# Kernel tuning notes

Hardware: AMD Instinct MI355X
Metric: run time of the kernel (lower is better)

Reference implementation:

```python
import jax, jax.numpy as jnp
import numpy as np

L_F, D_F = 32, 16      # fast window / hop
L_S, D_S = 32, 16      # slow window / hop
H = 32                 # SSM hidden dim
GH = 64                # GRU hidden dim
N_GRU = 4


def setup_inputs() -> dict:
    key = jax.random.key(0)
    ks = jax.random.split(key, 16)
    B, T = 2, 64000
    s = 0.1
    return {
        "x": jax.random.normal(ks[0], (B, T), jnp.float32),
        # slow branch input FC (1 -> GH), stored as (in, out)
        "slow_in_W": jax.random.normal(ks[1], (1, GH), jnp.float32) * s,
        "slow_in_b": jax.random.normal(ks[2], (GH,), jnp.float32) * s,
        # 4 stacked GRU layers, torch gate order [r, z, n], stored (in, 3*GH)
        "gru_Wih": jax.random.normal(ks[3], (N_GRU, GH, 3 * GH), jnp.float32) * s,
        "gru_Whh": jax.random.normal(ks[4], (N_GRU, GH, 3 * GH), jnp.float32) * s,
        "gru_bih": jax.random.normal(ks[5], (N_GRU, 3 * GH), jnp.float32) * s,
        "gru_bhh": jax.random.normal(ks[6], (N_GRU, 3 * GH), jnp.float32) * s,
        # slow branch output FC (GH -> GH)
        "slow_out_W": jax.random.normal(ks[7], (GH, GH), jnp.float32) * s,
        "slow_out_b": jax.random.normal(ks[8], (GH,), jnp.float32) * s,
        # slow_to_ssm (GH -> 2H)
        "s2s_W": jax.random.normal(ks[9], (GH, 2 * H), jnp.float32) * s,
        "s2s_b": jax.random.normal(ks[10], (2 * H,), jnp.float32) * s,
        # fast branch F_IN (1 -> H) and F_OUT (H -> 1)
        "fin_W": jax.random.normal(ks[11], (1, H), jnp.float32) * s,
        "fin_b": jax.random.normal(ks[12], (H,), jnp.float32) * s,
        "fout_W": jax.random.normal(ks[13], (H, 1), jnp.float32) * s,
        "fout_b": jax.random.normal(ks[14], (1,), jnp.float32) * s,
    }


def _forward(x, slow_in_W, slow_in_b, gru_Wih, gru_Whh, gru_bih, gru_bhh,
             slow_out_W, slow_out_b, s2s_W, s2s_b, fin_W, fin_b, fout_W, fout_b):
    B, T = x.shape
    nf = (T - L_F) // D_F + 1   # fast frame count
    ns = (T - L_S) // D_S + 1   # slow frame count
    fidx = jnp.arange(nf)[:, None] * D_F + jnp.arange(L_F)[None, :]  # (nf, L_F)
    sidx = jnp.arange(ns)[:, None] * D_S + jnp.arange(L_S)[None, :]  # (ns, L_S)
    frames = x[:, fidx]                                  # (B, nf, L_F)  == x.unfold

    BS = B * ns
    xs = x[:, sidx].reshape(BS, L_S, 1)
    h = jax.nn.relu(xs @ slow_in_W + slow_in_b)          # (BS, L_S, GH)
    for l in range(N_GRU):
        Whh, bhh = gru_Whh[l], gru_bhh[l]
        xg = h @ gru_Wih[l] + gru_bih[l]                 # (BS, L_S, 3GH)

        def step(hc, xg_t, Whh=Whh, bhh=bhh):
            hg = hc @ Whh + bhh
            r = jax.nn.sigmoid(xg_t[:, :GH] + hg[:, :GH])
            z = jax.nn.sigmoid(xg_t[:, GH:2 * GH] + hg[:, GH:2 * GH])
            n = jnp.tanh(xg_t[:, 2 * GH:] + r * hg[:, 2 * GH:])
            hn = (1.0 - z) * n + z * hc
            return hn, hn

        _, seq = jax.lax.scan(step, jnp.zeros((BS, GH), x.dtype), jnp.swapaxes(xg, 0, 1))
        h = jax.nn.relu(jnp.swapaxes(seq, 0, 1))         # (BS, L_S, GH)
    slow_feat = h[:, -1, :] @ slow_out_W + slow_out_b    # (BS, GH)

    # ---- modulation parameters ----
    eps = (slow_feat @ s2s_W + s2s_b).reshape(B, ns, 2 * H)
    A_s = jax.nn.sigmoid(eps[..., :H])                   # (B, ns, H)
    g_s = eps[..., H:]
    delta = D_S // D_F
    A_flat = jnp.repeat(A_s, delta, axis=1)[:, :nf].reshape(B * nf, H)
    g_flat = jnp.repeat(g_s, delta, axis=1)[:, :nf].reshape(B * nf, H)

    # ---- fast branch: diagonal SSM h_t = A*h_{t-1} + g * F_IN(x_t) ----
    ff = frames.reshape(B * nf, L_F, 1)
    x_emb = (ff @ fin_W + fin_b) * g_flat[:, None, :]    # (B*nf, L_F, H)

    def ssm_step(hc, xt):
        hn = A_flat * hc + xt
        return hn, hn

    _, hall = jax.lax.scan(ssm_step, jnp.zeros((B * nf, H), x.dtype),
                           jnp.swapaxes(x_emb, 0, 1))
    hall = jnp.swapaxes(hall, 0, 1)                      # (B*nf, L_F, H)
    s_hat = (hall @ fout_W + fout_b)[..., 0].reshape(B, nf, L_F)

    # ---- overlap-add (F.fold) ----
    out = jnp.zeros((B, T), x.dtype).at[:, fidx].add(s_hat)
    return out


def reference(x, slow_in_W, slow_in_b, gru_Wih, gru_Whh, gru_bih, gru_bhh,
              slow_out_W, slow_out_b, s2s_W, s2s_b, fin_W, fin_b, fout_W, fout_b):
    return _forward(x, slow_in_W, slow_in_b, gru_Wih, gru_Whh, gru_bih, gru_bhh,
                    slow_out_W, slow_out_b, s2s_W, s2s_b, fin_W, fin_b, fout_W, fout_b)
```

## Files before the change

kernel.cpp:

```cpp
#include <hip/hip_runtime.h>

#define GH 64
#define LS 32
#define HF 32
#define DS 16

#define NLOG2E -1.4426950408889634f
#define P2LOG2E 2.8853900817779268f

typedef short bf16x8 __attribute__((ext_vector_type(8)));
typedef float f32x4 __attribute__((ext_vector_type(4)));

#define MFMA16(a, b, c) __builtin_amdgcn_mfma_f32_16x16x32_bf16(a, b, c, 0, 0, 0)

__device__ __forceinline__ unsigned int f2bf_rne(float f) {
    unsigned int u = __float_as_uint(f);
    return (u + 0x7FFFu + ((u >> 16) & 1u)) >> 16;
}
__device__ __forceinline__ unsigned short f2bf_h(float f) {
    return (unsigned short)((__float_as_uint(f) + 0x8000u) >> 16);
}
__device__ __forceinline__ unsigned int pack_trunc(float v0, float v1) {
    return __builtin_amdgcn_perm(__float_as_uint(v1), __float_as_uint(v0),
                                 0x07060302u);
}
__device__ __forceinline__ bf16x8 as_frag(uint4 u) {
    union { uint4 a; bf16x8 b; } cv; cv.a = u; return cv.b;
}

__device__ __forceinline__ bf16x8 ld_afrag(const unsigned short* slot, int m,
                                           int quad, int half) {
    int b   = half * 4 + quad;
    int idx = (m << 6) + ((b ^ (m & 7)) << 3);
    return as_frag(*reinterpret_cast<const uint4*>(slot + idx));
}

__global__ __launch_bounds__(256) void prep_weights(
    const float* __restrict__ Wih, const float* __restrict__ Whh,
    const float* __restrict__ soW, const float* __restrict__ s2sW,
    unsigned short* __restrict__ wsW,
    float* __restrict__ out, int out_n)
{
    int gid = blockIdx.x * 256 + threadIdx.x;
    int nthreads = gridDim.x * 256;

    {
        float4* out4 = reinterpret_cast<float4*>(out);
        int n4 = out_n >> 2;
        for (int i = gid; i < n4; i += nthreads)
            out4[i] = make_float4(0.f, 0.f, 0.f, 0.f);
        int tail = out_n & 3;
        if (gid < tail) out[n4 * 4 + gid] = 0.0f;
    }

    if (gid >= 104 * 1024) return;

    float v;
    int dest;
    if (gid < 98304) {
        int g     = gid % 192;
        int r1    = gid / 192;
        int k     = r1 & 63;
        int r2    = r1 >> 6;
        int l     = r2 & 3;
        int which = r2 >> 2;
        int m3  = g / 64;
        int col = g - m3 * 64;
        const float* W = which ? Whh : Wih;
        v = W[(size_t)l * GH * 192 + k * 192 + g];
        v *= (m3 == 2) ? P2LOG2E : NLOG2E;
        int jt = col >> 4, c = col & 15;
        int mat  = which * 3 + m3;
        int rest = (l * 6 + mat) * 4 + jt;
        int kc = k >> 5, j = k & 7, lane = ((k >> 3) & 3) * 16 + c;
        dest = rest * 1024 + kc * 512 + lane * 8 + j;
    } else {
        int e   = gid - 98304;
        int col = e & 63;
        int k   = (e >> 6) & 63;
        int m2  = e >> 12;
        v = (m2 ? s2sW : soW)[k * 64 + col];
        if (m2 && col < 32) v *= NLOG2E;
        int jt = col >> 4, c = col & 15;
        int rest = 96 + m2 * 4 + jt;
        int kc = k >> 5, j = k & 7, lane = ((k >> 3) & 3) * 16 + c;
        dest = rest * 1024 + kc * 512 + lane * 8 + j;
    }
    wsW[dest] = (unsigned short)f2bf_rne(v);
}

__global__ __launch_bounds__(256, 2) void slowfast_fused(
    const float* __restrict__ x,
    const float* __restrict__ siW,  const float* __restrict__ sib,
    const float* __restrict__ bih,  const float* __restrict__ bhh,
    const float* __restrict__ sob,  const float* __restrict__ s2sb,
    const float* __restrict__ finW, const float* __restrict__ finb,
    const float* __restrict__ foutW, const float* __restrict__ foutb,
    const unsigned short* __restrict__ wsW,
    float* __restrict__ out,
    int T, int ns, int BS)
{
    __shared__ __align__(16) unsigned short hseq[LS * 16 * 64];
    __shared__ __align__(16) unsigned short hrec[2 * 16 * 64];
    __shared__ float xs[16 * 33];
    __shared__ float AG[16 * 65];

    const int tid  = threadIdx.x;
    const int lane = tid & 63;
    const int jt   = tid >> 6;
    const int c    = lane & 15;
    const int quad = lane >> 4;
    const int col  = jt * 16 + c;
    const int seqbase = blockIdx.x * 16;
    const uint4* wf = reinterpret_cast<const uint4*>(wsW);

    for (int p = tid; p < 512; p += 256) {
        int seq = p >> 5, t = p & 31;
        int q = seqbase + seq; if (q > BS - 1) q = BS - 1;
        int b  = (q >= ns) ? 1 : 0;
        int si = q - b * ns;
        xs[seq * 33 + t] = x[b * T + si * DS + t];
    }
    __syncthreads();

    {
        int chp = tid & 31;
        int grp = tid >> 5;
        int ch  = chp << 1;
        float w0 = siW[ch], w1 = siW[ch + 1];
        float b0 = sib[ch], b1 = sib[ch + 1];
        #pragma unroll 4
        for (int it = 0; it < 64; ++it) {
            int p = grp + (it << 3);
            int s = p >> 5, t = p & 31;
            float xv = xs[s * 33 + t];
            float v0 = fmaxf(fmaf(xv, w0, b0), 0.0f);
            float v1 = fmaxf(fmaf(xv, w1, b1), 0.0f);
            int idx = (t << 10) + (s << 6) + ((((ch >> 3) ^ (s & 7))) << 3) + (ch & 7);
            *reinterpret_cast<unsigned int*>(&hseq[idx]) = pack_trunc(v0, v1);
        }
    }

    int wIdx[4];
    #pragma unroll
    for (int i = 0; i < 4; ++i) {
        int row = quad * 4 + i;
        wIdx[i] = (row << 6) + ((((col >> 3) ^ (row & 7))) << 3) + (col & 7);
    }

    __syncthreads();

    bf16x8 a0 = ld_afrag(hseq, c, quad, 0);
    bf16x8 a1 = ld_afrag(hseq, c, quad, 1);

    for (int l = 0; l < 4; ++l) {
        bf16x8 BiR[2], BiZ[2], BiN[2], BhR[2], BhZ[2], BhN[2];
        #pragma unroll
        for (int kc = 0; kc < 2; ++kc) {
            int base = (l * 6 * 4 + jt) * 128 + kc * 64 + lane;
            BiR[kc] = as_frag(wf[base]);
            BiZ[kc] = as_frag(wf[base + 512]);
            BiN[kc] = as_frag(wf[base + 1024]);
            BhR[kc] = as_frag(wf[base + 1536]);
            BhZ[kc] = as_frag(wf[base + 2048]);
            BhN[kc] = as_frag(wf[base + 2560]);
        }
        float bRs  = NLOG2E  * (bih[l * 192 + col]      + bhh[l * 192 + col]);
        float bZs  = NLOG2E  * (bih[l * 192 + 64 + col] + bhh[l * 192 + 64 + col]);
        float bNIs = P2LOG2E * bih[l * 192 + 128 + col];
        float bNHs = P2LOG2E * bhh[l * 192 + 128 + col];
        const f32x4 vbR  = (f32x4){bRs,  bRs,  bRs,  bRs};
        const f32x4 vbZ  = (f32x4){bZs,  bZs,  bZs,  bZs};
        const f32x4 vbNI = (f32x4){bNIs, bNIs, bNIs, bNIs};
        const f32x4 vbNH = (f32x4){bNHs, bNHs, bNHs, bNHs};

        float hprev[4] = {0.0f, 0.0f, 0.0f, 0.0f};
        const bool storeSeq = (l != 3);

        #pragma unroll 2
        for (int t = 0; t < LS; ++t) {
            f32x4 aR  = MFMA16(a0, BiR[0], vbR);
            f32x4 aZ  = MFMA16(a0, BiZ[0], vbZ);
            f32x4 aNI = MFMA16(a0, BiN[0], vbNI);
            aR  = MFMA16(a1, BiR[1], aR);
            aZ  = MFMA16(a1, BiZ[1], aZ);
            aNI = MFMA16(a1, BiN[1], aNI);
            f32x4 aNH = vbNH;
            if (t > 0) {
                const unsigned short* hb = hrec + (((t - 1) & 1) << 10);
                bf16x8 h0 = ld_afrag(hb, c, quad, 0);
                bf16x8 h1 = ld_afrag(hb, c, quad, 1);
                aR  = MFMA16(h0, BhR[0], aR);
                aZ  = MFMA16(h0, BhZ[0], aZ);
                aNH = MFMA16(h0, BhN[0], aNH);
                aR  = MFMA16(h1, BhR[1], aR);
                aZ  = MFMA16(h1, BhZ[1], aZ);
                aNH = MFMA16(h1, BhN[1], aNH);
            }
            unsigned short* wb = hseq + (t << 10);
            unsigned short* wr = hrec + ((t & 1) << 10);
            const bool doSeq = storeSeq || (t == 31);
            #pragma unroll
            for (int i = 0; i < 4; ++i) {
                float r  = __builtin_amdgcn_rcpf(1.0f + __builtin_amdgcn_exp2f(aR[i]));
                float z  = __builtin_amdgcn_rcpf(1.0f + __builtin_amdgcn_exp2f(aZ[i]));
                float e  = __builtin_amdgcn_exp2f(fmaf(r, aNH[i], aNI[i]));
                float n  = fmaf(-2.0f, __builtin_amdgcn_rcpf(e + 1.0f), 1.0f);
                float hn = fmaf(z, hprev[i] - n, n);
                hprev[i] = hn;
                wr[wIdx[i]] = f2bf_h(hn);
                if (doSeq)
                    wb[wIdx[i]] = f2bf_h(fmaxf(hn, 0.0f));
            }
            const unsigned short* nb = hseq + (((t + 1) & 31) << 10);
            a0 = ld_afrag(nb, c, quad, 0);
            a1 = ld_afrag(nb, c, quad, 1);
            __syncthreads();
        }
    }

    {
        bf16x8 e0 = ld_afrag(hseq + (31 << 10), c, quad, 0);
        bf16x8 e1 = ld_afrag(hseq + (31 << 10), c, quad, 1);
        bf16x8 Bso[2], Bs2[2];
        #pragma unroll
        for (int kc = 0; kc < 2; ++kc) {
            Bso[kc] = as_frag(wf[(96 + jt)  * 128 + kc * 64 + lane]);
            Bs2[kc] = as_frag(wf[(100 + jt) * 128 + kc * 64 + lane]);
        }
        float sb = sob[col];
        f32x4 accS = (f32x4){sb, sb, sb, sb};
        accS = MFMA16(e0, Bso[0], accS);
        accS = MFMA16(e1, Bso[1], accS);
        #pragma unroll
        for (int i = 0; i < 4; ++i)
            hseq[wIdx[i]] = f2bf_h(accS[i]);
        __syncthreads();
        bf16x8 s0 = ld_afrag(hseq, c, quad, 0);
        bf16x8 s1 = ld_afrag(hseq, c, quad, 1);
        float eb = (jt < 2) ? NLOG2E * s2sb[col] : s2sb[col];
        f32x4 accE = (f32x4){eb, eb, eb, eb};
        accE = MFMA16(s0, Bs2[0], accE);
        accE = MFMA16(s1, Bs2[1], accE);
        #pragma unroll
        for (int i = 0; i < 4; ++i) {
            int row = quad * 4 + i;
            float v = accE[i];
            AG[row * 65 + col] = (jt < 2)
                ? __builtin_amdgcn_rcpf(1.0f + __builtin_amdgcn_exp2f(v)) : v;
        }
    }
    __syncthreads();
    {
        int fch = tid & 31;
        float Gfw = finW[fch], Gbw = finb[fch], cFo = foutW[fch], cfb = foutb[0];
        #pragma unroll
        for (int half = 0; half < 2; ++half) {
            int frame = half * 8 + (tid >> 5);
            int q = seqbase + frame;
            if (q < BS) {
                int b  = (q >= ns) ? 1 : 0;
                int fi = q - b * ns;
                float cA = AG[frame * 65 + fch];
                float cG = AG[frame * 65 + 32 + fch];
                float Gf = Gfw * cG;
                float Gb = Gbw * cG;
                float h = 0.0f;
                const float* xrow = xs + frame * 33;
                float* op = out + (size_t)b * T + fi * DS;
                #pragma unroll 1
                for (int t = 0; t < LS; ++t) {
                    h = fmaf(cA, h, fmaf(xrow[t], Gf, Gb));
                    float s = h * cFo;
                    s += __shfl_xor(s, 1);
                    s += __shfl_xor(s, 2);
                    s += __shfl_xor(s, 4);
                    s += __shfl_xor(s, 8);
                    s += __shfl_xor(s, 16);
                    if (fch == 0) atomicAdd(&op[t], s + cfb);
                }
            }
        }
    }
}

extern "C" void kernel_launch(void* const* d_in, const int* in_sizes, int n_in,
                              void* d_out, int out_size, void* d_ws, size_t ws_size,
                              hipStream_t stream)
{
    (void)n_in; (void)ws_size;
    const float* x     = (const float*)d_in[0];
    const float* siW   = (const float*)d_in[1];
    const float* sib   = (const float*)d_in[2];
    const float* Wih   = (const float*)d_in[3];
    const float* Whh   = (const float*)d_in[4];
    const float* bih   = (const float*)d_in[5];
    const float* bhh   = (const float*)d_in[6];
    const float* soW   = (const float*)d_in[7];
    const float* sob   = (const float*)d_in[8];
    const float* s2sW  = (const float*)d_in[9];
    const float* s2sb  = (const float*)d_in[10];
    const float* finW  = (const float*)d_in[11];
    const float* finb  = (const float*)d_in[12];
    const float* foutW = (const float*)d_in[13];
    const float* foutb = (const float*)d_in[14];

    int T  = in_sizes[0] / 2;
    int ns = (T - LS) / DS + 1;
    int BS = 2 * ns;

    unsigned short* wsW = (unsigned short*)d_ws;

    prep_weights<<<dim3(416), dim3(256), 0, stream>>>(
        Wih, Whh, soW, s2sW, wsW, (float*)d_out, out_size);

    slowfast_fused<<<dim3((BS + 15) / 16), dim3(256), 0, stream>>>(
        x, siW, sib, bih, bhh, sob, s2sb, finW, finb, foutW, foutb,
        wsW, (float*)d_out, T, ns, BS);
}
```

Baseline: 172.6 us.

## Move GRU sequence buffer from LDS to global workspace for higher occupancy

Adds a templated path that keeps the per-block 32-step hidden-sequence buffer (64 KB) in global workspace memory instead of shared memory, which frees LDS so the launch bound can request 4 blocks per CU instead of 2. The last-layer conditional store is removed, so every step is written. The cost is that each recurrent step now reads and writes activations through the global/L2 path instead of LDS, adding latency on the serial recurrence. It falls back to the LDS version when the workspace is too small.

```diff
diff --git a/kernel.cpp b/kernel.cpp
--- a/kernel.cpp
+++ b/kernel.cpp
@@ -28,7 +28,8 @@
     union { uint4 a; bf16x8 b; } cv; cv.a = u; return cv.b;
 }
 
-__device__ __forceinline__ bf16x8 ld_afrag(const unsigned short* slot, int m,
+template <typename P>
+__device__ __forceinline__ bf16x8 ld_afrag(const P* slot, int m,
                                            int quad, int half) {
     int b   = half * 4 + quad;
     int idx = (m << 6) + ((b ^ (m & 7)) << 3);
@@ -89,7 +90,8 @@
     wsW[dest] = (unsigned short)f2bf_rne(v);
 }
 
-__global__ __launch_bounds__(256, 2) void slowfast_fused(
+template <bool GHSEQ>
+__global__ __launch_bounds__(256, GHSEQ ? 4 : 2) void slowfast_fused(
     const float* __restrict__ x,
     const float* __restrict__ siW,  const float* __restrict__ sib,
     const float* __restrict__ bih,  const float* __restrict__ bhh,
@@ -97,10 +99,11 @@
     const float* __restrict__ finW, const float* __restrict__ finb,
     const float* __restrict__ foutW, const float* __restrict__ foutb,
     const unsigned short* __restrict__ wsW,
+    unsigned short* __restrict__ hsg,
     float* __restrict__ out,
     int T, int ns, int BS)
 {
-    __shared__ __align__(16) unsigned short hseq[LS * 16 * 64];
+    __shared__ __align__(16) unsigned short hseq_l[GHSEQ ? 64 : LS * 16 * 64];
     __shared__ __align__(16) unsigned short hrec[2 * 16 * 64];
     __shared__ float xs[16 * 33];
     __shared__ float AG[16 * 65];
@@ -113,6 +116,9 @@
     const int col  = jt * 16 + c;
     const int seqbase = blockIdx.x * 16;
     const uint4* wf = reinterpret_cast<const uint4*>(wsW);
+
+    unsigned short* hseq = GHSEQ ? (hsg + (size_t)blockIdx.x * (LS * 16 * 64))
+                                 : hseq_l;
 
     for (int p = tid; p < 512; p += 256) {
         int seq = p >> 5, t = p & 31;
@@ -175,7 +181,6 @@
         const f32x4 vbNH = (f32x4){bNHs, bNHs, bNHs, bNHs};
 
         float hprev[4] = {0.0f, 0.0f, 0.0f, 0.0f};
-        const bool storeSeq = (l != 3);
 
         #pragma unroll 2
         for (int t = 0; t < LS; ++t) {
@@ -199,7 +204,6 @@
             }
             unsigned short* wb = hseq + (t << 10);
             unsigned short* wr = hrec + ((t & 1) << 10);
-            const bool doSeq = storeSeq || (t == 31);
             #pragma unroll
             for (int i = 0; i < 4; ++i) {
                 float r  = __builtin_amdgcn_rcpf(1.0f + __builtin_amdgcn_exp2f(aR[i]));
@@ -209,8 +213,7 @@
                 float hn = fmaf(z, hprev[i] - n, n);
                 hprev[i] = hn;
                 wr[wIdx[i]] = f2bf_h(hn);
-                if (doSeq)
-                    wb[wIdx[i]] = f2bf_h(fmaxf(hn, 0.0f));
+                wb[wIdx[i]] = f2bf_h(fmaxf(hn, 0.0f));
             }
             const unsigned short* nb = hseq + (((t + 1) & 31) << 10);
             a0 = ld_afrag(nb, c, quad, 0);
@@ -288,7 +291,7 @@
                               void* d_out, int out_size, void* d_ws, size_t ws_size,
                               hipStream_t stream)
 {
-    (void)n_in; (void)ws_size;
+    (void)n_in;
     const float* x     = (const float*)d_in[0];
     const float* siW   = (const float*)d_in[1];
     const float* sib   = (const float*)d_in[2];
@@ -308,13 +311,23 @@
     int T  = in_sizes[0] / 2;
     int ns = (T - LS) / DS + 1;
     int BS = 2 * ns;
+    int nblocks = (BS + 15) / 16;
 
     unsigned short* wsW = (unsigned short*)d_ws;
 
     prep_weights<<<dim3(416), dim3(256), 0, stream>>>(
         Wih, Whh, soW, s2sW, wsW, (float*)d_out, out_size);
 
-    slowfast_fused<<<dim3((BS + 15) / 16), dim3(256), 0, stream>>>(
-        x, siW, sib, bih, bhh, sob, s2sb, finW, finb, foutW, foutb,
-        wsW, (float*)d_out, T, ns, BS);
-}
+    size_t need = (size_t)(4 << 20) + (size_t)nblocks * (LS * 16 * 64 * 2);
+    if (ws_size >= need) {
+        unsigned short* hsg =
+            (unsigned short*)((char*)d_ws + (4 << 20));
+        slowfast_fused<true><<<dim3(nblocks), dim3(256), 0, stream>>>(
+            x, siW, sib, bih, bhh, sob, s2sb, finW, finb, foutW, foutb,
+            wsW, hsg, (float*)d_out, T, ns, BS);
+    } else {
+        slowfast_fused<false><<<dim3(nblocks), dim3(256), 0, stream>>>(
+            x, siW, sib, bih, bhh, sob, s2sb, finW, finb, foutW, foutb,
+            wsW, nullptr, (float*)d_out, T, ns, BS);
+    }
+}
```

After: 201.0 us. +16.5%, slower.

## Pipeline four GRU layers as a wavefront across waves in 1024-thread blocks

Applied to the files above, without the earlier changes.

The four stacked GRU layers, previously run one after another by the same four waves, now each get four waves of a 1024-thread block. They run as a diagonal wavefront: layer l handles timestep tau-l, and activations pass through double-buffered LDS boundary tiles. This cuts the serial step count from 128 to 35 barrier-separated steps and drops the full 32-step hseq buffer, so LDS use shrinks. The input FC is computed per step directly into MFMA fragments. In exchange each barrier now syncs 16 waves, waves idle at the pipeline ends, and per-CU occupancy and register limits change with the larger block.

```diff
diff --git a/kernel.cpp b/kernel.cpp
--- a/kernel.cpp
+++ b/kernel.cpp
@@ -89,7 +89,7 @@
     wsW[dest] = (unsigned short)f2bf_rne(v);
 }
 
-__global__ __launch_bounds__(256, 2) void slowfast_fused(
+__global__ __launch_bounds__(1024, 4) void slowfast_fused(
     const float* __restrict__ x,
     const float* __restrict__ siW,  const float* __restrict__ sib,
     const float* __restrict__ bih,  const float* __restrict__ bhh,
@@ -100,46 +100,55 @@
     float* __restrict__ out,
     int T, int ns, int BS)
 {
-    __shared__ __align__(16) unsigned short hseq[LS * 16 * 64];
-    __shared__ __align__(16) unsigned short hrec[2 * 16 * 64];
+    __shared__ __align__(16) unsigned short bnd[3 * 2 * 1024];
+    __shared__ __align__(16) unsigned short hrec[4 * 2 * 1024];
+    __shared__ __align__(16) unsigned short hfin[1024];
     __shared__ float xs[16 * 33];
     __shared__ float AG[16 * 65];
+    __shared__ __align__(16) float swS[64], sbS[64];
 
     const int tid  = threadIdx.x;
     const int lane = tid & 63;
-    const int jt   = tid >> 6;
+    const int w    = tid >> 6;
+    const int l    = w >> 2;
+    const int jt   = w & 3;
     const int c    = lane & 15;
     const int quad = lane >> 4;
     const int col  = jt * 16 + c;
     const int seqbase = blockIdx.x * 16;
     const uint4* wf = reinterpret_cast<const uint4*>(wsW);
 
-    for (int p = tid; p < 512; p += 256) {
-        int seq = p >> 5, t = p & 31;
+    if (tid < 512) {
+        int seq = tid >> 5, t = tid & 31;
         int q = seqbase + seq; if (q > BS - 1) q = BS - 1;
         int b  = (q >= ns) ? 1 : 0;
         int si = q - b * ns;
         xs[seq * 33 + t] = x[b * T + si * DS + t];
-    }
-    __syncthreads();
-
-    {
-        int chp = tid & 31;
-        int grp = tid >> 5;
-        int ch  = chp << 1;
-        float w0 = siW[ch], w1 = siW[ch + 1];
-        float b0 = sib[ch], b1 = sib[ch + 1];
-        #pragma unroll 4
-        for (int it = 0; it < 64; ++it) {
-            int p = grp + (it << 3);
-            int s = p >> 5, t = p & 31;
-            float xv = xs[s * 33 + t];
-            float v0 = fmaxf(fmaf(xv, w0, b0), 0.0f);
-            float v1 = fmaxf(fmaf(xv, w1, b1), 0.0f);
-            int idx = (t << 10) + (s << 6) + ((((ch >> 3) ^ (s & 7))) << 3) + (ch & 7);
-            *reinterpret_cast<unsigned int*>(&hseq[idx]) = pack_trunc(v0, v1);
-        }
-    }
+    } else if (tid < 576) {
+        int i = tid - 512;
+        swS[i] = siW[i];
+        sbS[i] = sib[i];
+    }
+
+    bf16x8 BiR[2], BiZ[2], BiN[2], BhR[2], BhZ[2], BhN[2];
+    #pragma unroll
+    for (int kc = 0; kc < 2; ++kc) {
+        int base = (l * 24 + jt) * 128 + kc * 64 + lane;
+        BiR[kc] = as_frag(wf[base]);
+        BiZ[kc] = as_frag(wf[base + 512]);
+        BiN[kc] = as_frag(wf[base + 1024]);
+        BhR[kc] = as_frag(wf[base + 1536]);
+        BhZ[kc] = as_frag(wf[base + 2048]);
+        BhN[kc] = as_frag(wf[base + 2560]);
+    }
+    float bRs  = NLOG2E  * (bih[l * 192 + col]      + bhh[l * 192 + col]);
+    float bZs  = NLOG2E  * (bih[l * 192 + 64 + col] + bhh[l * 192 + 64 + col]);
+    float bNIs = P2LOG2E * bih[l * 192 + 128 + col];
+    float bNHs = P2LOG2E * bhh[l * 192 + 128 + col];
+    const f32x4 vbR  = (f32x4){bRs,  bRs,  bRs,  bRs};
+    const f32x4 vbZ  = (f32x4){bZs,  bZs,  bZs,  bZs};
+    const f32x4 vbNI = (f32x4){bNIs, bNIs, bNIs, bNIs};
+    const f32x4 vbNH = (f32x4){bNHs, bNHs, bNHs, bNHs};
 
     int wIdx[4];
     #pragma unroll
@@ -148,96 +157,108 @@
         wIdx[i] = (row << 6) + ((((col >> 3) ^ (row & 7))) << 3) + (col & 7);
     }
 
+    float hprev[4] = {0.0f, 0.0f, 0.0f, 0.0f};
+    const float4* sw4 = reinterpret_cast<const float4*>(swS);
+    const float4* sb4 = reinterpret_cast<const float4*>(sbS);
+
+    #pragma unroll 1
+    for (int tau = 0; tau < 35; ++tau) {
+        __syncthreads();
+        int t = tau - l;
+        if (t < 0 || t >= 32) continue;
+
+        bf16x8 a0, a1;
+        if (l == 0) {
+            float xv = xs[c * 33 + t];
+            float4 wA = sw4[quad * 2],     wB = sw4[quad * 2 + 1];
+            float4 bA = sb4[quad * 2],     bB = sb4[quad * 2 + 1];
+            float4 wC = sw4[8 + quad * 2], wD = sw4[8 + quad * 2 + 1];
+            float4 bC = sb4[8 + quad * 2], bD = sb4[8 + quad * 2 + 1];
+            uint4 u;
+            u.x = pack_trunc(fmaxf(fmaf(xv, wA.x, bA.x), 0.f),
+                             fmaxf(fmaf(xv, wA.y, bA.y), 0.f));
+            u.y = pack_trunc(fmaxf(fmaf(xv, wA.z, bA.z), 0.f),
+                             fmaxf(fmaf(xv, wA.w, bA.w), 0.f));
+            u.z = pack_trunc(fmaxf(fmaf(xv, wB.x, bB.x), 0.f),
+                             fmaxf(fmaf(xv, wB.y, bB.y), 0.f));
+            u.w = pack_trunc(fmaxf(fmaf(xv, wB.z, bB.z), 0.f),
+                             fmaxf(fmaf(xv, wB.w, bB.w), 0.f));
+            a0 = as_frag(u);
+            u.x = pack_trunc(fmaxf(fmaf(xv, wC.x, bC.x), 0.f),
+                             fmaxf(fmaf(xv, wC.y, bC.y), 0.f));
+            u.y = pack_trunc(fmaxf(fmaf(xv, wC.z, bC.z), 0.f),
+                             fmaxf(fmaf(xv, wC.w, bC.w), 0.f));
+            u.z = pack_trunc(fmaxf(fmaf(xv, wD.x, bD.x), 0.f),
+                             fmaxf(fmaf(xv, wD.y, bD.y), 0.f));
+            u.w = pack_trunc(fmaxf(fmaf(xv, wD.z, bD.z), 0.f),
+                             fmaxf(fmaf(xv, wD.w, bD.w), 0.f));
+            a1 = as_frag(u);
+        } else {
+            const unsigned short* src = bnd + (((l - 1) << 1) + (t & 1)) * 1024;
+            a0 = ld_afrag(src, c, quad, 0);
+            a1 = ld_afrag(src, c, quad, 1);
+        }
+
+        f32x4 aR  = MFMA16(a0, BiR[0], vbR);
+        f32x4 aZ  = MFMA16(a0, BiZ[0], vbZ);
+        f32x4 aNI = MFMA16(a0, BiN[0], vbNI);
+        aR  = MFMA16(a1, BiR[1], aR);
+        aZ  = MFMA16(a1, BiZ[1], aZ);
+        aNI = MFMA16(a1, BiN[1], aNI);
+        f32x4 aNH = vbNH;
+        if (t > 0) {
+            const unsigned short* hb = hrec + ((l << 1) + ((t - 1) & 1)) * 1024;
+            bf16x8 h0 = ld_afrag(hb, c, quad, 0);
+            bf16x8 h1 = ld_afrag(hb, c, quad, 1);
+            aR  = MFMA16(h0, BhR[0], aR);
+            aZ  = MFMA16(h0, BhZ[0], aZ);
+            aNH = MFMA16(h0, BhN[0], aNH);
+            aR  = MFMA16(h1, BhR[1], aR);
+            aZ  = MFMA16(h1, BhZ[1], aZ);
+            aNH = MFMA16(h1, BhN[1], aNH);
+        }
+        unsigned short* wr = hrec + ((l << 1) + (t & 1)) * 1024;
+        unsigned short* wb = (l < 3) ? (bnd + ((l << 1) + (t & 1)) * 1024)
+                                     : hfin;
+        #pragma unroll
+        for (int i = 0; i < 4; ++i) {
+            float r  = __builtin_amdgcn_rcpf(1.0f + __builtin_amdgcn_exp2f(aR[i]));
+            float z  = __builtin_amdgcn_rcpf(1.0f + __builtin_amdgcn_exp2f(aZ[i]));
+            float e  = __builtin_amdgcn_exp2f(fmaf(r, aNH[i], aNI[i]));
+            float n  = fmaf(-2.0f, __builtin_amdgcn_rcpf(e + 1.0f), 1.0f);
+            float hn = fmaf(z, hprev[i] - n, n);
+            hprev[i] = hn;
+            wr[wIdx[i]] = f2bf_h(hn);
+            wb[wIdx[i]] = f2bf_h(fmaxf(hn, 0.0f));
+        }
+    }
     __syncthreads();
 
-    bf16x8 a0 = ld_afrag(hseq, c, quad, 0);
-    bf16x8 a1 = ld_afrag(hseq, c, quad, 1);
-
-    for (int l = 0; l < 4; ++l) {
-        bf16x8 BiR[2], BiZ[2], BiN[2], BhR[2], BhZ[2], BhN[2];
-        #pragma unroll
-        for (int kc = 0; kc < 2; ++kc) {
-            int base = (l * 6 * 4 + jt) * 128 + kc * 64 + lane;
-            BiR[kc] = as_frag(wf[base]);
-            BiZ[kc] = as_frag(wf[base + 512]);
-            BiN[kc] = as_frag(wf[base + 1024]);
-            BhR[kc] = as_frag(wf[base + 1536]);
-            BhZ[kc] = as_frag(wf[base + 2048]);
-            BhN[kc] = as_frag(wf[base + 2560]);
-        }
-        float bRs  = NLOG2E  * (bih[l * 192 + col]      + bhh[l * 192 + col]);
-        float bZs  = NLOG2E  * (bih[l * 192 + 64 + col] + bhh[l * 192 + 64 + col]);
-        float bNIs = P2LOG2E * bih[l * 192 + 128 + col];
-        float bNHs = P2LOG2E * bhh[l * 192 + 128 + col];
-        const f32x4 vbR  = (f32x4){bRs,  bRs,  bRs,  bRs};
-        const f32x4 vbZ  = (f32x4){bZs,  bZs,  bZs,  bZs};
-        const f32x4 vbNI = (f32x4){bNIs, bNIs, bNIs, bNIs};
-        const f32x4 vbNH = (f32x4){bNHs, bNHs, bNHs, bNHs};
-
-        float hprev[4] = {0.0f, 0.0f, 0.0f, 0.0f};
-        const bool storeSeq = (l != 3);
-
-        #pragma unroll 2
-        for (int t = 0; t < LS; ++t) {
-            f32x4 aR  = MFMA16(a0, BiR[0], vbR);
-            f32x4 aZ  = MFMA16(a0, BiZ[0], vbZ);
-            f32x4 aNI = MFMA16(a0, BiN[0], vbNI);
-            aR  = MFMA16(a1, BiR[1], aR);
-            aZ  = MFMA16(a1, BiZ[1], aZ);
-            aNI = MFMA16(a1, BiN[1], aNI);
-            f32x4 aNH = vbNH;
-            if (t > 0) {
-                const unsigned short* hb = hrec + (((t - 1) & 1) << 10);
-                bf16x8 h0 = ld_afrag(hb, c, quad, 0);
-                bf16x8 h1 = ld_afrag(hb, c, quad, 1);
-                aR  = MFMA16(h0, BhR[0], aR);
-                aZ  = MFMA16(h0, BhZ[0], aZ);
-                aNH = MFMA16(h0, BhN[0], aNH);
-                aR  = MFMA16(h1, BhR[1], aR);
-                aZ  = MFMA16(h1, BhZ[1], aZ);
-                aNH = MFMA16(h1, BhN[1], aNH);
-            }
-            unsigned short* wb = hseq + (t << 10);
-            unsigned short* wr = hrec + ((t & 1) << 10);
-            const bool doSeq = storeSeq || (t == 31);
-            #pragma unroll
-            for (int i = 0; i < 4; ++i) {
-                float r  = __builtin_amdgcn_rcpf(1.0f + __builtin_amdgcn_exp2f(aR[i]));
-                float z  = __builtin_amdgcn_rcpf(1.0f + __builtin_amdgcn_exp2f(aZ[i]));
-                float e  = __builtin_amdgcn_exp2f(fmaf(r, aNH[i], aNI[i]));
-                float n  = fmaf(-2.0f, __builtin_amdgcn_rcpf(e + 1.0f), 1.0f);
-                float hn = fmaf(z, hprev[i] - n, n);
-                hprev[i] = hn;
-                wr[wIdx[i]] = f2bf_h(hn);
-                if (doSeq)
-                    wb[wIdx[i]] = f2bf_h(fmaxf(hn, 0.0f));
-            }
-            const unsigned short* nb = hseq + (((t + 1) & 31) << 10);
-            a0 = ld_afrag(nb, c, quad, 0);
-            a1 = ld_afrag(nb, c, quad, 1);
-            __syncthreads();
-        }
-    }
-
-    {
-        bf16x8 e0 = ld_afrag(hseq + (31 << 10), c, quad, 0);
-        bf16x8 e1 = ld_afrag(hseq + (31 << 10), c, quad, 1);
-        bf16x8 Bso[2], Bs2[2];
+    f32x4 accS;
+    bf16x8 Bso[2], Bs2[2];
+    if (w < 4) {
+        bf16x8 e0 = ld_afrag(hfin, c, quad, 0);
+        bf16x8 e1 = ld_afrag(hfin, c, quad, 1);
         #pragma unroll
         for (int kc = 0; kc < 2; ++kc) {
             Bso[kc] = as_frag(wf[(96 + jt)  * 128 + kc * 64 + lane]);
             Bs2[kc] = as_frag(wf[(100 + jt) * 128 + kc * 64 + lane]);
         }
         float sb = sob[col];
-        f32x4 accS = (f32x4){sb, sb, sb, sb};
+        accS = (f32x4){sb, sb, sb, sb};
         accS = MFMA16(e0, Bso[0], accS);
         accS = MFMA16(e1, Bso[1], accS);
+    }
+    __syncthreads();
+    if (w < 4) {
         #pragma unroll
         for (int i = 0; i < 4; ++i)
-            hseq[wIdx[i]] = f2bf_h(accS[i]);
-        __syncthreads();
-        bf16x8 s0 = ld_afrag(hseq, c, quad, 0);
-        bf16x8 s1 = ld_afrag(hseq, c, quad, 1);
+            hfin[wIdx[i]] = f2bf_h(accS[i]);
+    }
+    __syncthreads();
+    if (w < 4) {
+        bf16x8 s0 = ld_afrag(hfin, c, quad, 0);
+        bf16x8 s1 = ld_afrag(hfin, c, quad, 1);
         float eb = (jt < 2) ? NLOG2E * s2sb[col] : s2sb[col];
         f32x4 accE = (f32x4){eb, eb, eb, eb};
         accE = MFMA16(s0, Bs2[0], accE);
@@ -251,34 +272,32 @@
         }
     }
     __syncthreads();
-    {
-        int fch = tid & 31;
-        float Gfw = finW[fch], Gbw = finb[fch], cFo = foutW[fch], cfb = foutb[0];
-        #pragma unroll
-        for (int half = 0; half < 2; ++half) {
-            int frame = half * 8 + (tid >> 5);
-            int q = seqbase + frame;
-            if (q < BS) {
-                int b  = (q >= ns) ? 1 : 0;
-                int fi = q - b * ns;
-                float cA = AG[frame * 65 + fch];
-                float cG = AG[frame * 65 + 32 + fch];
-                float Gf = Gfw * cG;
-                float Gb = Gbw * cG;
-                float h = 0.0f;
-                const float* xrow = xs + frame * 33;
-                float* op = out + (size_t)b * T + fi * DS;
-                #pragma unroll 1
-                for (int t = 0; t < LS; ++t) {
-                    h = fmaf(cA, h, fmaf(xrow[t], Gf, Gb));
-                    float s = h * cFo;
-                    s += __shfl_xor(s, 1);
-                    s += __shfl_xor(s, 2);
-                    s += __shfl_xor(s, 4);
-                    s += __shfl_xor(s, 8);
-                    s += __shfl_xor(s, 16);
-                    if (fch == 0) atomicAdd(&op[t], s + cfb);
-                }
+    if (tid < 512) {
+        int fch   = tid & 31;
+        int frame = tid >> 5;
+        int q = seqbase + frame;
+        if (q < BS) {
+            float Gfw = finW[fch], Gbw = finb[fch];
+            float cFo = foutW[fch], cfb = foutb[0];
+            int b  = (q >= ns) ? 1 : 0;
+            int fi = q - b * ns;
+            float cA = AG[frame * 65 + fch];
+            float cG = AG[frame * 65 + 32 + fch];
+            float Gf = Gfw * cG;
+            float Gb = Gbw * cG;
+            float h = 0.0f;
+            const float* xrow = xs + frame * 33;
+            float* op = out + (size_t)b * T + fi * DS;
+            #pragma unroll 1
+            for (int t = 0; t < LS; ++t) {
+                h = fmaf(cA, h, fmaf(xrow[t], Gf, Gb));
+                float s = h * cFo;
+                s += __shfl_xor(s, 1);
+                s += __shfl_xor(s, 2);
+                s += __shfl_xor(s, 4);
+                s += __shfl_xor(s, 8);
+                s += __shfl_xor(s, 16);
+                if (fch == 0) atomicAdd(&op[t], s + cfb);
             }
         }
     }
@@ -308,13 +327,14 @@
     int T  = in_sizes[0] / 2;
     int ns = (T - LS) / DS + 1;
     int BS = 2 * ns;
+    int nblocks = (BS + 15) / 16;
 
     unsigned short* wsW = (unsigned short*)d_ws;
 
     prep_weights<<<dim3(416), dim3(256), 0, stream>>>(
         Wih, Whh, soW, s2sW, wsW, (float*)d_out, out_size);
 
-    slowfast_fused<<<dim3((BS + 15) / 16), dim3(256), 0, stream>>>(
+    slowfast_fused<<<dim3(nblocks), dim3(1024), 0, stream>>>(
         x, siW, sib, bih, bhh, sob, s2sb, finW, finb, foutW, foutb,
         wsW, (float*)d_out, T, ns, BS);
 }
```

After: 179.3 us. +3.9%, slower.

## Process two 16-sequence tiles per block to interleave independent GRU chains

Applied to the files above, without the earlier changes.

Each block now handles 32 slow sequences as two independent 16-row tiles (A and B), issuing their MFMAs and gate math interleaved so one tile's dependent chain can hide the other's latency. Doing this halves the number of blocks and per-step barriers per sequence, and the recurrent weight fragments are reused for twice the rows. In exchange it doubles LDS and register use, lowers occupancy (launch bounds change from 2 to 1), and always writes the layer-3 sequence to LDS even though only the last step is needed.

```diff
diff --git a/kernel.cpp b/kernel.cpp
--- a/kernel.cpp
+++ b/kernel.cpp
@@ -89,7 +89,25 @@
     wsW[dest] = (unsigned short)f2bf_rne(v);
 }
 
-__global__ __launch_bounds__(256, 2) void slowfast_fused(
+__device__ __forceinline__ void gate4(const f32x4& aR, const f32x4& aZ,
+                                      const f32x4& aNI, const f32x4& aNH,
+                                      float* hprev, unsigned short* wr,
+                                      unsigned short* wb, const int* wIdx)
+{
+    #pragma unroll
+    for (int i = 0; i < 4; ++i) {
+        float r  = __builtin_amdgcn_rcpf(1.0f + __builtin_amdgcn_exp2f(aR[i]));
+        float z  = __builtin_amdgcn_rcpf(1.0f + __builtin_amdgcn_exp2f(aZ[i]));
+        float e  = __builtin_amdgcn_exp2f(fmaf(r, aNH[i], aNI[i]));
+        float n  = fmaf(-2.0f, __builtin_amdgcn_rcpf(e + 1.0f), 1.0f);
+        float hn = fmaf(z, hprev[i] - n, n);
+        hprev[i] = hn;
+        wr[wIdx[i]] = f2bf_h(hn);
+        wb[wIdx[i]] = f2bf_h(fmaxf(hn, 0.0f));
+    }
+}
+
+__global__ __launch_bounds__(256, 1) void slowfast_fused(
     const float* __restrict__ x,
     const float* __restrict__ siW,  const float* __restrict__ sib,
     const float* __restrict__ bih,  const float* __restrict__ bhh,
@@ -100,10 +118,13 @@
     float* __restrict__ out,
     int T, int ns, int BS)
 {
-    __shared__ __align__(16) unsigned short hseq[LS * 16 * 64];
-    __shared__ __align__(16) unsigned short hrec[2 * 16 * 64];
-    __shared__ float xs[16 * 33];
-    __shared__ float AG[16 * 65];
+    __shared__ __align__(16) unsigned short hseq[2 * LS * 16 * 64];
+    __shared__ __align__(16) unsigned short hrec[2 * 2 * 16 * 64];
+    __shared__ float xs[32 * 33];
+    __shared__ float AG[32 * 65];
+
+    unsigned short* hseqA = hseq;
+    unsigned short* hseqB = hseq + LS * 16 * 64;
 
     const int tid  = threadIdx.x;
     const int lane = tid & 63;
@@ -111,10 +132,10 @@
     const int c    = lane & 15;
     const int quad = lane >> 4;
     const int col  = jt * 16 + c;
-    const int seqbase = blockIdx.x * 16;
+    const int seqbase = blockIdx.x * 32;
     const uint4* wf = reinterpret_cast<const uint4*>(wsW);
 
-    for (int p = tid; p < 512; p += 256) {
+    for (int p = tid; p < 1024; p += 256) {
         int seq = p >> 5, t = p & 31;
         int q = seqbase + seq; if (q > BS - 1) q = BS - 1;
         int b  = (q >= ns) ? 1 : 0;
@@ -133,11 +154,15 @@
         for (int it = 0; it < 64; ++it) {
             int p = grp + (it << 3);
             int s = p >> 5, t = p & 31;
+            int idx = (t << 10) + (s << 6) + ((((ch >> 3) ^ (s & 7))) << 3) + (ch & 7);
             float xv = xs[s * 33 + t];
-            float v0 = fmaxf(fmaf(xv, w0, b0), 0.0f);
-            float v1 = fmaxf(fmaf(xv, w1, b1), 0.0f);
-            int idx = (t << 10) + (s << 6) + ((((ch >> 3) ^ (s & 7))) << 3) + (ch & 7);
-            *reinterpret_cast<unsigned int*>(&hseq[idx]) = pack_trunc(v0, v1);
+            *reinterpret_cast<unsigned int*>(&hseqA[idx]) =
+                pack_trunc(fmaxf(fmaf(xv, w0, b0), 0.0f),
+                           fmaxf(fmaf(xv, w1, b1), 0.0f));
+            float xw = xs[(s + 16) * 33 + t];
+            *reinterpret_cast<unsigned int*>(&hseqB[idx]) =
+                pack_trunc(fmaxf(fmaf(xw, w0, b0), 0.0f),
+                           fmaxf(fmaf(xw, w1, b1), 0.0f));
         }
     }
 
@@ -150,8 +175,10 @@
 
     __syncthreads();
 
-    bf16x8 a0 = ld_afrag(hseq, c, quad, 0);
-    bf16x8 a1 = ld_afrag(hseq, c, quad, 1);
+    bf16x8 aA0 = ld_afrag(hseqA, c, quad, 0);
+    bf16x8 aA1 = ld_afrag(hseqA, c, quad, 1);
+    bf16x8 aB0 = ld_afrag(hseqB, c, quad, 0);
+    bf16x8 aB1 = ld_afrag(hseqB, c, quad, 1);
 
     for (int l = 0; l < 4; ++l) {
         bf16x8 BiR[2], BiZ[2], BiN[2], BhR[2], BhZ[2], BhN[2];
@@ -174,54 +201,60 @@
         const f32x4 vbNI = (f32x4){bNIs, bNIs, bNIs, bNIs};
         const f32x4 vbNH = (f32x4){bNHs, bNHs, bNHs, bNHs};
 
-        float hprev[4] = {0.0f, 0.0f, 0.0f, 0.0f};
-        const bool storeSeq = (l != 3);
+        float hprevA[4] = {0.0f, 0.0f, 0.0f, 0.0f};
+        float hprevB[4] = {0.0f, 0.0f, 0.0f, 0.0f};
 
         #pragma unroll 2
         for (int t = 0; t < LS; ++t) {
-            f32x4 aR  = MFMA16(a0, BiR[0], vbR);
-            f32x4 aZ  = MFMA16(a0, BiZ[0], vbZ);
-            f32x4 aNI = MFMA16(a0, BiN[0], vbNI);
-            aR  = MFMA16(a1, BiR[1], aR);
-            aZ  = MFMA16(a1, BiZ[1], aZ);
-            aNI = MFMA16(a1, BiN[1], aNI);
-            f32x4 aNH = vbNH;
+            f32x4 aRA  = MFMA16(aA0, BiR[0], vbR);
+            f32x4 aRB  = MFMA16(aB0, BiR[0], vbR);
+            f32x4 aZA  = MFMA16(aA0, BiZ[0], vbZ);
+            f32x4 aZB  = MFMA16(aB0, BiZ[0], vbZ);
+            f32x4 aNIA = MFMA16(aA0, BiN[0], vbNI);
+            f32x4 aNIB = MFMA16(aB0, BiN[0], vbNI);
+            aRA  = MFMA16(aA1, BiR[1], aRA);
+            aRB  = MFMA16(aB1, BiR[1], aRB);
+            aZA  = MFMA16(aA1, BiZ[1], aZA);
+            aZB  = MFMA16(aB1, BiZ[1], aZB);
+            aNIA = MFMA16(aA1, BiN[1], aNIA);
+            aNIB = MFMA16(aB1, BiN[1], aNIB);
+            f32x4 aNHA = vbNH;
+            f32x4 aNHB = vbNH;
             if (t > 0) {
-                const unsigned short* hb = hrec + (((t - 1) & 1) << 10);
-                bf16x8 h0 = ld_afrag(hb, c, quad, 0);
-                bf16x8 h1 = ld_afrag(hb, c, quad, 1);
-                aR  = MFMA16(h0, BhR[0], aR);
-                aZ  = MFMA16(h0, BhZ[0], aZ);
-                aNH = MFMA16(h0, BhN[0], aNH);
-                aR  = MFMA16(h1, BhR[1], aR);
-                aZ  = MFMA16(h1, BhZ[1], aZ);
-                aNH = MFMA16(h1, BhN[1], aNH);
+                const unsigned short* hbA = hrec + (((t - 1) & 1) << 10);
+                const unsigned short* hbB = hbA + 2048;
+                bf16x8 h0A = ld_afrag(hbA, c, quad, 0);
+                bf16x8 h1A = ld_afrag(hbA, c, quad, 1);
+                bf16x8 h0B = ld_afrag(hbB, c, quad, 0);
+                bf16x8 h1B = ld_afrag(hbB, c, quad, 1);
+                aRA  = MFMA16(h0A, BhR[0], aRA);
+                aRB  = MFMA16(h0B, BhR[0], aRB);
+                aZA  = MFMA16(h0A, BhZ[0], aZA);
+                aZB  = MFMA16(h0B, BhZ[0], aZB);
+                aNHA = MFMA16(h0A, BhN[0], aNHA);
+                aNHB = MFMA16(h0B, BhN[0], aNHB);
+                aRA  = MFMA16(h1A, BhR[1], aRA);
+                aRB  = MFMA16(h1B, BhR[1], aRB);
+                aZA  = MFMA16(h1A, BhZ[1], aZA);
+                aZB  = MFMA16(h1B, BhZ[1], aZB);
+                aNHA = MFMA16(h1A, BhN[1], aNHA);
+                aNHB = MFMA16(h1B, BhN[1], aNHB);
             }
-            unsigned short* wb = hseq + (t << 10);
-            unsigned short* wr = hrec + ((t & 1) << 10);
-            const bool doSeq = storeSeq || (t == 31);
-            #pragma unroll
-            for (int i = 0; i < 4; ++i) {
-                float r  = __builtin_amdgcn_rcpf(1.0f + __builtin_amdgcn_exp2f(aR[i]));
-                float z  = __builtin_amdgcn_rcpf(1.0f + __builtin_amdgcn_exp2f(aZ[i]));
-                float e  = __builtin_amdgcn_exp2f(fmaf(r, aNH[i], aNI[i]));
-                float n  = fmaf(-2.0f, __builtin_amdgcn_rcpf(e + 1.0f), 1.0f);
-                float hn = fmaf(z, hprev[i] - n, n);
-                hprev[i] = hn;
-                wr[wIdx[i]] = f2bf_h(hn);
-                if (doSeq)
-                    wb[wIdx[i]] = f2bf_h(fmaxf(hn, 0.0f));
-            }
-            const unsigned short* nb = hseq + (((t + 1) & 31) << 10);
-            a0 = ld_afrag(nb, c, quad, 0);
-            a1 = ld_afrag(nb, c, quad, 1);
+            unsigned short* wrA = hrec + ((t & 1) << 10);
+            unsigned short* wrB = wrA + 2048;
+            gate4(aRA, aZA, aNIA, aNHA, hprevA, wrA, hseqA + (t << 10), wIdx);
+            gate4(aRB, aZB, aNIB, aNHB, hprevB, wrB, hseqB + (t << 10), wIdx);
+            const unsigned short* nbA = hseqA + (((t + 1) & 31) << 10);
+            const unsigned short* nbB = hseqB + (((t + 1) & 31) << 10);
+            aA0 = ld_afrag(nbA, c, quad, 0);
+            aA1 = ld_afrag(nbA, c, quad, 1);
+            aB0 = ld_afrag(nbB, c, quad, 0);
+            aB1 = ld_afrag(nbB, c, quad, 1);
             __syncthreads();
         }
     }
 
     {
-        bf16x8 e0 = ld_afrag(hseq + (31 << 10), c, quad, 0);
-        bf16x8 e1 = ld_afrag(hseq + (31 << 10), c, quad, 1);
         bf16x8 Bso[2], Bs2[2];
         #pragma unroll
         for (int kc = 0; kc < 2; ++kc) {
@@ -229,25 +262,42 @@
             Bs2[kc] = as_frag(wf[(100 + jt) * 128 + kc * 64 + lane]);
         }
         float sb = sob[col];
-        f32x4 accS = (f32x4){sb, sb, sb, sb};
-        accS = MFMA16(e0, Bso[0], accS);
-        accS = MFMA16(e1, Bso[1], accS);
-        #pragma unroll
-        for (int i = 0; i < 4; ++i)
-            hseq[wIdx[i]] = f2bf_h(accS[i]);
+        bf16x8 eA0 = ld_afrag(hseqA + (31 << 10), c, quad, 0);
+        bf16x8 eA1 = ld_afrag(hseqA + (31 << 10), c, quad, 1);
+        bf16x8 eB0 = ld_afrag(hseqB + (31 << 10), c, quad, 0);
+        bf16x8 eB1 = ld_afrag(hseqB + (31 << 10), c, quad, 1);
+        f32x4 accSA = (f32x4){sb, sb, sb, sb};
+        f32x4 accSB = (f32x4){sb, sb, sb, sb};
+        accSA = MFMA16(eA0, Bso[0], accSA);
+        accSB = MFMA16(eB0, Bso[0], accSB);
+        accSA = MFMA16(eA1, Bso[1], accSA);
+        accSB = MFMA16(eB1, Bso[1], accSB);
+        #pragma unroll
+        for (int i = 0; i < 4; ++i) {
+            hseqA[wIdx[i]] = f2bf_h(accSA[i]);
+            hseqB[wIdx[i]] = f2bf_h(accSB[i]);
+        }
         __syncthreads();
-        bf16x8 s0 = ld_afrag(hseq, c, quad, 0);
-        bf16x8 s1 = ld_afrag(hseq, c, quad, 1);
+        bf16x8 sA0 = ld_afrag(hseqA, c, quad, 0);
+        bf16x8 sA1 = ld_afrag(hseqA, c, quad, 1);
+        bf16x8 sB0 = ld_afrag(hseqB, c, quad, 0);
+        bf16x8 sB1 = ld_afrag(hseqB, c, quad, 1);
         float eb = (jt < 2) ? NLOG2E * s2sb[col] : s2sb[col];
-        f32x4 accE = (f32x4){eb, eb, eb, eb};
-        accE = MFMA16(s0, Bs2[0], accE);
-        accE = MFMA16(s1, Bs2[1], accE);
+        f32x4 accEA = (f32x4){eb, eb, eb, eb};
+        f32x4 accEB = (f32x4){eb, eb, eb, eb};
+        accEA = MFMA16(sA0, Bs2[0], accEA);
+        accEB = MFMA16(sB0, Bs2[0], accEB);
+        accEA = MFMA16(sA1, Bs2[1], accEA);
+        accEB = MFMA16(sB1, Bs2[1], accEB);
         #pragma unroll
         for (int i = 0; i < 4; ++i) {
             int row = quad * 4 + i;
-            float v = accE[i];
+            float vA = accEA[i];
+            float vB = accEB[i];
             AG[row * 65 + col] = (jt < 2)
-                ? __builtin_amdgcn_rcpf(1.0f + __builtin_amdgcn_exp2f(v)) : v;
+                ? __builtin_amdgcn_rcpf(1.0f + __builtin_amdgcn_exp2f(vA)) : vA;
+            AG[(row + 16) * 65 + col] = (jt < 2)
+                ? __builtin_amdgcn_rcpf(1.0f + __builtin_amdgcn_exp2f(vB)) : vB;
         }
     }
     __syncthreads();
@@ -255,8 +305,8 @@
         int fch = tid & 31;
         float Gfw = finW[fch], Gbw = finb[fch], cFo = foutW[fch], cfb = foutb[0];
         #pragma unroll
-        for (int half = 0; half < 2; ++half) {
-            int frame = half * 8 + (tid >> 5);
+        for (int qtr = 0; qtr < 4; ++qtr) {
+            int frame = qtr * 8 + (tid >> 5);
             int q = seqbase + frame;
             if (q < BS) {
                 int b  = (q >= ns) ? 1 : 0;
@@ -308,13 +358,14 @@
     int T  = in_sizes[0] / 2;
     int ns = (T - LS) / DS + 1;
     int BS = 2 * ns;
+    int nblocks = (BS + 31) / 32;
 
     unsigned short* wsW = (unsigned short*)d_ws;
 
     prep_weights<<<dim3(416), dim3(256), 0, stream>>>(
         Wih, Whh, soW, s2sW, wsW, (float*)d_out, out_size);
 
-    slowfast_fused<<<dim3((BS + 15) / 16), dim3(256), 0, stream>>>(
+    slowfast_fused<<<dim3(nblocks), dim3(256), 0, stream>>>(
         x, siW, sib, bih, bhh, sob, s2sb, finW, finb, foutW, foutb,
         wsW, (float*)d_out, T, ns, BS);
 }
```

Result: slower. 211.6 us (+22.6%).
